# Kernel optimization log

Measured on AMD Instinct MI355X. Metric: run time of the kernel, lower is better.

Reference implementation:

```python
import jax, jax.numpy as jnp
import numpy as np

SIGMA = 0.1
GAMMA = 1.0 / (SIGMA * SIGMA)  # keops-style gauss kernel: exp(-|x-y|^2 / sigma^2)
B, N, D = 1, 8192, 3


def setup_inputs() -> dict:
    key = jax.random.key(0)
    k1, k2 = jax.random.split(key)
    control_points = jax.random.uniform(k1, (B, N, D), dtype=jnp.float32)
    mom = jax.random.normal(k2, (B, N, D), dtype=jnp.float32) * 0.1
    return {"mom": mom, "control_points": control_points}


def _pairwise_dist2(x, y):
    # x:[B,N,D], y:[B,M,D] -> [B,N,M] squared distances (no N x M x D intermediate)
    x2 = jnp.sum(x * x, -1)  # [B,N]
    y2 = jnp.sum(y * y, -1)  # [B,M]
    xy = jnp.einsum('bnd,bmd->bnm', x, y)
    return x2[:, :, None] + y2[:, None, :] - 2.0 * xy


def gauss_kernel(x, y, b):
    # K(x,y) b : [B,N,d]
    K = jnp.exp(-GAMMA * _pairwise_dist2(x, y))  # [B,N,M]
    return jnp.einsum('bnm,bmd->bnd', K, b)


def gauss_grad_kernel(p, x):
    # dH/dx_i = sum_j d/dx_i[exp(-g|x_i-x_j|^2)] <p_i,p_j>
    #         = -2g * sum_j K_ij <p_i,p_j> (x_i - x_j)
    K = jnp.exp(-GAMMA * _pairwise_dist2(x, x))        # [B,N,N]
    W = K * jnp.einsum('bnd,bmd->bnm', p, p)           # [B,N,N] weighted by <p_i,p_j>
    row_sum = jnp.sum(W, -1)                           # [B,N]
    Wx = jnp.einsum('bnm,bmd->bnd', W, x)              # [B,N,D]
    return (-2.0 * GAMMA) * (x * row_sum[:, :, None] - Wx)


def reference(mom, control_points):
    # variational_evolve: (dp/dt, dx/dt)
    dmom = -gauss_grad_kernel(mom, control_points)
    dx = gauss_kernel(control_points, control_points, mom)
    return (dmom, dx)
```

## Files before the change

### kernel.cpp

```cpp
#include <hip/hip_runtime.h>


#define TPB 256
#define ITILE 2
constexpr float GAMMA_C = 100.0f;
constexpr float LOG2E_C = 1.4426950408889634f;
constexpr float SB_C    = 2.0f * GAMMA_C * LOG2E_C;
constexpr float SC_C    = -GAMMA_C * LOG2E_C;
constexpr float LN2_C   = 0.69314718055994531f;

__global__ __launch_bounds__(TPB, 4) void lddmm_partial(
    const float* __restrict__ mom, const float* __restrict__ xpt,
    float* __restrict__ ws, int N, int SEG, int JT) {
  extern __shared__ float4 smem[];
  float4* sA = smem;
  float4* sP = smem + JT;
  const int tid = threadIdx.x;
  const int seg = blockIdx.y;

  for (int t = tid; t < JT; t += TPB) {
    const int j = seg * JT + t;
    const float bx = xpt[3*j], by = xpt[3*j+1], bz = xpt[3*j+2];
    sA[t] = make_float4(SB_C*bx, SB_C*by, SB_C*bz,
                        SC_C * fmaf(bx, bx, fmaf(by, by, bz*bz)));
    sP[t] = make_float4(mom[3*j], mom[3*j+1], mom[3*j+2], 0.f);
  }
  __syncthreads();

  const int i0 = blockIdx.x * (TPB * ITILE) + tid;
  const int i1 = i0 + TPB;

  const float x0 = xpt[3*i0], y0 = xpt[3*i0+1], z0 = xpt[3*i0+2];
  const float p0x = mom[3*i0], p0y = mom[3*i0+1], p0z = mom[3*i0+2];
  const float c0 = SC_C * fmaf(x0, x0, fmaf(y0, y0, z0*z0));
  const float x1 = xpt[3*i1], y1 = xpt[3*i1+1], z1 = xpt[3*i1+2];
  const float p1x = mom[3*i1], p1y = mom[3*i1+1], p1z = mom[3*i1+2];
  const float c1 = SC_C * fmaf(x1, x1, fmaf(y1, y1, z1*z1));

  float a0=0.f, wx0=0.f, wy0=0.f, wz0=0.f, gx0=0.f, gy0=0.f, gz0=0.f;
  float a1=0.f, wx1=0.f, wy1=0.f, wz1=0.f, gx1=0.f, gy1=0.f, gz1=0.f;

#pragma unroll 4
  for (int t = 0; t < JT; ++t) {
    const float4 A = sA[t];
    const float4 P = sP[t];
    {
      const float arg = fmaf(A.x, x0, fmaf(A.y, y0, fmaf(A.z, z0, c0 + A.w)));
      const float K   = __builtin_amdgcn_exp2f(arg);
      const float dot = fmaf(P.x, p0x, fmaf(P.y, p0y, P.z * p0z));
      const float w   = K * dot;
      a0 += w;
      wx0 = fmaf(w, A.x, wx0); wy0 = fmaf(w, A.y, wy0); wz0 = fmaf(w, A.z, wz0);
      gx0 = fmaf(K, P.x, gx0); gy0 = fmaf(K, P.y, gy0); gz0 = fmaf(K, P.z, gz0);
    }
    {
      const float arg = fmaf(A.x, x1, fmaf(A.y, y1, fmaf(A.z, z1, c1 + A.w)));
      const float K   = __builtin_amdgcn_exp2f(arg);
      const float dot = fmaf(P.x, p1x, fmaf(P.y, p1y, P.z * p1z));
      const float w   = K * dot;
      a1 += w;
      wx1 = fmaf(w, A.x, wx1); wy1 = fmaf(w, A.y, wy1); wz1 = fmaf(w, A.z, wz1);
      gx1 = fmaf(K, P.x, gx1); gy1 = fmaf(K, P.y, gy1); gz1 = fmaf(K, P.z, gz1);
    }
  }

  const size_t SN = (size_t)SEG * N;
  float* p = ws + (size_t)seg * N;
  p[0*SN+i0] = a0;  p[0*SN+i1] = a1;
  p[1*SN+i0] = wx0; p[1*SN+i1] = wx1;
  p[2*SN+i0] = wy0; p[2*SN+i1] = wy1;
  p[3*SN+i0] = wz0; p[3*SN+i1] = wz1;
  p[4*SN+i0] = gx0; p[4*SN+i1] = gx1;
  p[5*SN+i0] = gy0; p[5*SN+i1] = gy1;
  p[6*SN+i0] = gz0; p[6*SN+i1] = gz1;
}

__global__ __launch_bounds__(TPB) void lddmm_reduce(
    const float* __restrict__ ws, float* __restrict__ R, int N, int SEG) {
  const int i = blockIdx.x * TPB + threadIdx.x;
  const int c = blockIdx.y;
  const float* src = ws + (size_t)c * SEG * N + i;
  float s0 = 0.f, s1 = 0.f, s2 = 0.f, s3 = 0.f;
  int s = 0;
  for (; s + 4 <= SEG; s += 4) {
    s0 += src[(size_t)(s+0)*N]; s1 += src[(size_t)(s+1)*N];
    s2 += src[(size_t)(s+2)*N]; s3 += src[(size_t)(s+3)*N];
  }
  for (; s < SEG; ++s) s0 += src[(size_t)s*N];
  R[(size_t)c * N + i] = (s0 + s1) + (s2 + s3);
}

__global__ __launch_bounds__(TPB) void lddmm_finalize(
    const float* __restrict__ R, const float* __restrict__ xpt,
    float* __restrict__ out, int N) {
  const int i = blockIdx.x * TPB + threadIdx.x;
  const float A  = R[i];
  const float WX = R[(size_t)1*N+i], WY = R[(size_t)2*N+i], WZ = R[(size_t)3*N+i];
  const float GX = R[(size_t)4*N+i], GY = R[(size_t)5*N+i], GZ = R[(size_t)6*N+i];
  const float xi = xpt[3*i], yi = xpt[3*i+1], zi = xpt[3*i+2];
  const float TGA = 2.0f * GAMMA_C * A;
  out[3*i+0] = fmaf(TGA, xi, -LN2_C * WX);
  out[3*i+1] = fmaf(TGA, yi, -LN2_C * WY);
  out[3*i+2] = fmaf(TGA, zi, -LN2_C * WZ);
  out[3*N + 3*i + 0] = GX;
  out[3*N + 3*i + 1] = GY;
  out[3*N + 3*i + 2] = GZ;
}

__global__ __launch_bounds__(TPB) void lddmm_atomic(
    const float* __restrict__ mom, const float* __restrict__ xpt,
    float* __restrict__ out, int N) {
  const int i  = blockIdx.x * TPB + threadIdx.x;
  const int jb = blockIdx.y * TPB;
  __shared__ float4 sA[TPB], sP[TPB];
  {
    const int j = jb + threadIdx.x;
    const float bx = xpt[3*j], by = xpt[3*j+1], bz = xpt[3*j+2];
    sA[threadIdx.x] = make_float4(SB_C*bx, SB_C*by, SB_C*bz,
                                  SC_C * fmaf(bx, bx, fmaf(by, by, bz*bz)));
    sP[threadIdx.x] = make_float4(mom[3*j], mom[3*j+1], mom[3*j+2], 0.f);
  }
  __syncthreads();
  const float xi = xpt[3*i], yi = xpt[3*i+1], zi = xpt[3*i+2];
  const float pxi = mom[3*i], pyi = mom[3*i+1], pzi = mom[3*i+2];
  const float ci = SC_C * fmaf(xi, xi, fmaf(yi, yi, zi*zi));
  float a=0.f, wx=0.f, wy=0.f, wz=0.f, gx=0.f, gy=0.f, gz=0.f;
#pragma unroll 4
  for (int t = 0; t < TPB; ++t) {
    const float4 A = sA[t], P = sP[t];
    const float arg = fmaf(A.x, xi, fmaf(A.y, yi, fmaf(A.z, zi, ci + A.w)));
    const float K   = __builtin_amdgcn_exp2f(arg);
    const float dot = fmaf(P.x, pxi, fmaf(P.y, pyi, P.z * pzi));
    const float w   = K * dot;
    a += w;
    wx = fmaf(w, A.x, wx); wy = fmaf(w, A.y, wy); wz = fmaf(w, A.z, wz);
    gx = fmaf(K, P.x, gx); gy = fmaf(K, P.y, gy); gz = fmaf(K, P.z, gz);
  }
  const float TGA = 2.0f * GAMMA_C * a;
  atomicAdd(&out[3*i+0], fmaf(TGA, xi, -LN2_C * wx));
  atomicAdd(&out[3*i+1], fmaf(TGA, yi, -LN2_C * wy));
  atomicAdd(&out[3*i+2], fmaf(TGA, zi, -LN2_C * wz));
  atomicAdd(&out[3*N+3*i+0], gx);
  atomicAdd(&out[3*N+3*i+1], gy);
  atomicAdd(&out[3*N+3*i+2], gz);
}

extern "C" void kernel_launch(void* const* d_in, const int* in_sizes, int n_in,
                              void* d_out, int out_size, void* d_ws, size_t ws_size,
                              hipStream_t stream) {
  const float* mom = (const float*)d_in[0];
  const float* xpt = (const float*)d_in[1];
  float* out = (float*)d_out;
  const int N = in_sizes[0] / 3;

  auto need = [&](int s) { return (size_t)(7*s + 7) * (size_t)N * sizeof(float); };
  int SEG = 64;
  while (SEG > 2 && need(SEG) > ws_size) SEG >>= 1;

  if (need(SEG) <= ws_size) {
    const int JT = N / SEG;
    float* wsf = (float*)d_ws;
    float* R   = wsf + (size_t)7 * SEG * N;
    const size_t shmem = (size_t)JT * 2 * sizeof(float4);
    dim3 gA(N / (TPB * ITILE), SEG);
    lddmm_partial<<<gA, TPB, shmem, stream>>>(mom, xpt, wsf, N, SEG, JT);
    dim3 gB(N / TPB, 7);
    lddmm_reduce<<<gB, TPB, 0, stream>>>(wsf, R, N, SEG);
    lddmm_finalize<<<N / TPB, TPB, 0, stream>>>(R, xpt, out, N);
  } else {
    hipMemsetAsync(d_out, 0, (size_t)out_size * sizeof(float), stream);
    dim3 grid(N / TPB, N / TPB);
    lddmm_atomic<<<grid, TPB, 0, stream>>>(mom, xpt, out, N);
  }
}
```

Baseline: 97.04 us.

## Precompute packed point tables once and read them from global instead of LDS

Adds a pre-pass kernel that builds the scaled position/norm and momentum float4 tables once in workspace. The partial kernel drops its per-block LDS staging and barrier and reads these tables directly through the cache with uniform addresses. SEG is raised to 128 and launch bounds to 8 waves per SIMD to increase occupancy. The cost is an extra kernel launch, a larger partial-sum workspace and reduction, and inner-loop operands that now come from global/scalar loads instead of LDS.

Result: slower. 104.9 us (+8.1%).

```diff
diff --git a/kernel.cpp b/kernel.cpp
--- a/kernel.cpp
+++ b/kernel.cpp
@@ -9,23 +9,25 @@
 constexpr float SC_C    = -GAMMA_C * LOG2E_C;
 constexpr float LN2_C   = 0.69314718055994531f;
 
-__global__ __launch_bounds__(TPB, 4) void lddmm_partial(
+__global__ __launch_bounds__(TPB) void lddmm_pre(
+    const float* __restrict__ mom, const float* __restrict__ xpt,
+    float4* __restrict__ At, float4* __restrict__ Pt, int N) {
+  const int j = blockIdx.x * TPB + threadIdx.x;
+  if (j < N) {
+    const float bx = xpt[3*j], by = xpt[3*j+1], bz = xpt[3*j+2];
+    At[j] = make_float4(SB_C*bx, SB_C*by, SB_C*bz,
+                        SC_C * fmaf(bx, bx, fmaf(by, by, bz*bz)));
+    Pt[j] = make_float4(mom[3*j], mom[3*j+1], mom[3*j+2], 0.f);
+  }
+}
+
+__global__ __launch_bounds__(TPB, 8) void lddmm_partial(
+    const float4* __restrict__ At, const float4* __restrict__ Pt,
     const float* __restrict__ mom, const float* __restrict__ xpt,
     float* __restrict__ ws, int N, int SEG, int JT) {
-  extern __shared__ float4 smem[];
-  float4* sA = smem;
-  float4* sP = smem + JT;
   const int tid = threadIdx.x;
   const int seg = blockIdx.y;
-
-  for (int t = tid; t < JT; t += TPB) {
-    const int j = seg * JT + t;
-    const float bx = xpt[3*j], by = xpt[3*j+1], bz = xpt[3*j+2];
-    sA[t] = make_float4(SB_C*bx, SB_C*by, SB_C*bz,
-                        SC_C * fmaf(bx, bx, fmaf(by, by, bz*bz)));
-    sP[t] = make_float4(mom[3*j], mom[3*j+1], mom[3*j+2], 0.f);
-  }
-  __syncthreads();
+  const int jb  = seg * JT;
 
   const int i0 = blockIdx.x * (TPB * ITILE) + tid;
   const int i1 = i0 + TPB;
@@ -42,8 +44,8 @@
 
 #pragma unroll 4
   for (int t = 0; t < JT; ++t) {
-    const float4 A = sA[t];
-    const float4 P = sP[t];
+    const float4 A = At[jb + t];
+    const float4 P = Pt[jb + t];
     {
       const float arg = fmaf(A.x, x0, fmaf(A.y, y0, fmaf(A.z, z0, c0 + A.w)));
       const float K   = __builtin_amdgcn_exp2f(arg);
@@ -153,17 +155,22 @@
   float* out = (float*)d_out;
   const int N = in_sizes[0] / 3;
 
-  auto need = [&](int s) { return (size_t)(7*s + 7) * (size_t)N * sizeof(float); };
-  int SEG = 64;
+  auto need = [&](int s) {
+    return (size_t)(8 + 7*s + 7) * (size_t)N * sizeof(float);
+  };
+  int SEG = 128;
   while (SEG > 2 && need(SEG) > ws_size) SEG >>= 1;
 
   if (need(SEG) <= ws_size) {
     const int JT = N / SEG;
-    float* wsf = (float*)d_ws;
-    float* R   = wsf + (size_t)7 * SEG * N;
-    const size_t shmem = (size_t)JT * 2 * sizeof(float4);
+    float4* At = (float4*)d_ws;
+    float4* Pt = At + N;
+    float*  wsf = (float*)(Pt + N);
+    float*  R   = wsf + (size_t)7 * SEG * N;
+
+    lddmm_pre<<<N / TPB, TPB, 0, stream>>>(mom, xpt, At, Pt, N);
     dim3 gA(N / (TPB * ITILE), SEG);
-    lddmm_partial<<<gA, TPB, shmem, stream>>>(mom, xpt, wsf, N, SEG, JT);
+    lddmm_partial<<<gA, TPB, 0, stream>>>(At, Pt, mom, xpt, wsf, N, SEG, JT);
     dim3 gB(N / TPB, 7);
     lddmm_reduce<<<gB, TPB, 0, stream>>>(wsf, R, N, SEG);
     lddmm_finalize<<<N / TPB, TPB, 0, stream>>>(R, xpt, out, N);
```

## Broadcast source points via readlane instead of LDS and widen i-tile to four

Applied to the files above, without the earlier changes.

The partial kernel no longer stages the j-points in shared memory. Each lane of a wavefront loads one j-point into registers, and the loop broadcasts it to the whole wave with readlane across 64 iterations, removing LDS traffic and the block barrier. Each thread now accumulates four i-points instead of two, for more instruction-level parallelism and more reuse of each broadcast. The cost is fixing the segment count at N/64, which doubles the partial-sum workspace and the traffic the reduce kernel must read. If the workspace is too small for that, the code falls back to the slow atomic path.

Measured after the change: 108.0 us. 11.3% more time.

```diff
diff --git a/kernel.cpp b/kernel.cpp
--- a/kernel.cpp
+++ b/kernel.cpp
@@ -2,77 +2,101 @@
 
 
 #define TPB 256
-#define ITILE 2
+#define ITILE 4
 constexpr float GAMMA_C = 100.0f;
 constexpr float LOG2E_C = 1.4426950408889634f;
 constexpr float SB_C    = 2.0f * GAMMA_C * LOG2E_C;
 constexpr float SC_C    = -GAMMA_C * LOG2E_C;
 constexpr float LN2_C   = 0.69314718055994531f;
 
+static __device__ __forceinline__ float rl(float v, int l) {
+  return __int_as_float(__builtin_amdgcn_readlane(__float_as_int(v), l));
+}
+
 __global__ __launch_bounds__(TPB, 4) void lddmm_partial(
     const float* __restrict__ mom, const float* __restrict__ xpt,
-    float* __restrict__ ws, int N, int SEG, int JT) {
-  extern __shared__ float4 smem[];
-  float4* sA = smem;
-  float4* sP = smem + JT;
-  const int tid = threadIdx.x;
-  const int seg = blockIdx.y;
+    float* __restrict__ ws, int N, int SEG) {
+  const int tid  = threadIdx.x;
+  const int lane = tid & 63;
+  const int seg  = blockIdx.y;
+  const int j    = seg * 64 + lane;
 
-  for (int t = tid; t < JT; t += TPB) {
-    const int j = seg * JT + t;
-    const float bx = xpt[3*j], by = xpt[3*j+1], bz = xpt[3*j+2];
-    sA[t] = make_float4(SB_C*bx, SB_C*by, SB_C*bz,
-                        SC_C * fmaf(bx, bx, fmaf(by, by, bz*bz)));
-    sP[t] = make_float4(mom[3*j], mom[3*j+1], mom[3*j+2], 0.f);
-  }
-  __syncthreads();
+  const float bx = xpt[3*j], by = xpt[3*j+1], bz = xpt[3*j+2];
+  const float ax = SB_C * bx, ay = SB_C * by, az = SB_C * bz;
+  const float ac = SC_C * fmaf(bx, bx, fmaf(by, by, bz * bz));
+  const float qx = mom[3*j], qy = mom[3*j+1], qz = mom[3*j+2];
 
   const int i0 = blockIdx.x * (TPB * ITILE) + tid;
-  const int i1 = i0 + TPB;
-
+  const int i1 = i0 + TPB, i2 = i0 + 2*TPB, i3 = i0 + 3*TPB;
   const float x0 = xpt[3*i0], y0 = xpt[3*i0+1], z0 = xpt[3*i0+2];
+  const float x1 = xpt[3*i1], y1 = xpt[3*i1+1], z1 = xpt[3*i1+2];
+  const float x2 = xpt[3*i2], y2 = xpt[3*i2+1], z2 = xpt[3*i2+2];
+  const float x3 = xpt[3*i3], y3 = xpt[3*i3+1], z3 = xpt[3*i3+2];
   const float p0x = mom[3*i0], p0y = mom[3*i0+1], p0z = mom[3*i0+2];
+  const float p1x = mom[3*i1], p1y = mom[3*i1+1], p1z = mom[3*i1+2];
+  const float p2x = mom[3*i2], p2y = mom[3*i2+1], p2z = mom[3*i2+2];
+  const float p3x = mom[3*i3], p3y = mom[3*i3+1], p3z = mom[3*i3+2];
   const float c0 = SC_C * fmaf(x0, x0, fmaf(y0, y0, z0*z0));
-  const float x1 = xpt[3*i1], y1 = xpt[3*i1+1], z1 = xpt[3*i1+2];
-  const float p1x = mom[3*i1], p1y = mom[3*i1+1], p1z = mom[3*i1+2];
   const float c1 = SC_C * fmaf(x1, x1, fmaf(y1, y1, z1*z1));
+  const float c2 = SC_C * fmaf(x2, x2, fmaf(y2, y2, z2*z2));
+  const float c3 = SC_C * fmaf(x3, x3, fmaf(y3, y3, z3*z3));
 
   float a0=0.f, wx0=0.f, wy0=0.f, wz0=0.f, gx0=0.f, gy0=0.f, gz0=0.f;
   float a1=0.f, wx1=0.f, wy1=0.f, wz1=0.f, gx1=0.f, gy1=0.f, gz1=0.f;
+  float a2=0.f, wx2=0.f, wy2=0.f, wz2=0.f, gx2=0.f, gy2=0.f, gz2=0.f;
+  float a3=0.f, wx3=0.f, wy3=0.f, wz3=0.f, gx3=0.f, gy3=0.f, gz3=0.f;
 
-#pragma unroll 4
-  for (int t = 0; t < JT; ++t) {
-    const float4 A = sA[t];
-    const float4 P = sP[t];
+#pragma unroll 8
+  for (int l = 0; l < 64; ++l) {
+    const float Ax = rl(ax, l), Ay = rl(ay, l), Az = rl(az, l), Aw = rl(ac, l);
+    const float Px = rl(qx, l), Py = rl(qy, l), Pz = rl(qz, l);
     {
-      const float arg = fmaf(A.x, x0, fmaf(A.y, y0, fmaf(A.z, z0, c0 + A.w)));
+      const float arg = fmaf(Ax, x0, fmaf(Ay, y0, fmaf(Az, z0, c0 + Aw)));
       const float K   = __builtin_amdgcn_exp2f(arg);
-      const float dot = fmaf(P.x, p0x, fmaf(P.y, p0y, P.z * p0z));
+      const float dot = fmaf(Px, p0x, fmaf(Py, p0y, Pz * p0z));
       const float w   = K * dot;
       a0 += w;
-      wx0 = fmaf(w, A.x, wx0); wy0 = fmaf(w, A.y, wy0); wz0 = fmaf(w, A.z, wz0);
-      gx0 = fmaf(K, P.x, gx0); gy0 = fmaf(K, P.y, gy0); gz0 = fmaf(K, P.z, gz0);
+      wx0 = fmaf(w, Ax, wx0); wy0 = fmaf(w, Ay, wy0); wz0 = fmaf(w, Az, wz0);
+      gx0 = fmaf(K, Px, gx0); gy0 = fmaf(K, Py, gy0); gz0 = fmaf(K, Pz, gz0);
     }
     {
-      const float arg = fmaf(A.x, x1, fmaf(A.y, y1, fmaf(A.z, z1, c1 + A.w)));
+      const float arg = fmaf(Ax, x1, fmaf(Ay, y1, fmaf(Az, z1, c1 + Aw)));
       const float K   = __builtin_amdgcn_exp2f(arg);
-      const float dot = fmaf(P.x, p1x, fmaf(P.y, p1y, P.z * p1z));
+      const float dot = fmaf(Px, p1x, fmaf(Py, p1y, Pz * p1z));
       const float w   = K * dot;
       a1 += w;
-      wx1 = fmaf(w, A.x, wx1); wy1 = fmaf(w, A.y, wy1); wz1 = fmaf(w, A.z, wz1);
-      gx1 = fmaf(K, P.x, gx1); gy1 = fmaf(K, P.y, gy1); gz1 = fmaf(K, P.z, gz1);
+      wx1 = fmaf(w, Ax, wx1); wy1 = fmaf(w, Ay, wy1); wz1 = fmaf(w, Az, wz1);
+      gx1 = fmaf(K, Px, gx1); gy1 = fmaf(K, Py, gy1); gz1 = fmaf(K, Pz, gz1);
+    }
+    {
+      const float arg = fmaf(Ax, x2, fmaf(Ay, y2, fmaf(Az, z2, c2 + Aw)));
+      const float K   = __builtin_amdgcn_exp2f(arg);
+      const float dot = fmaf(Px, p2x, fmaf(Py, p2y, Pz * p2z));
+      const float w   = K * dot;
+      a2 += w;
+      wx2 = fmaf(w, Ax, wx2); wy2 = fmaf(w, Ay, wy2); wz2 = fmaf(w, Az, wz2);
+      gx2 = fmaf(K, Px, gx2); gy2 = fmaf(K, Py, gy2); gz2 = fmaf(K, Pz, gz2);
+    }
+    {
+      const float arg = fmaf(Ax, x3, fmaf(Ay, y3, fmaf(Az, z3, c3 + Aw)));
+      const float K   = __builtin_amdgcn_exp2f(arg);
+      const float dot = fmaf(Px, p3x, fmaf(Py, p3y, Pz * p3z));
+      const float w   = K * dot;
+      a3 += w;
+      wx3 = fmaf(w, Ax, wx3); wy3 = fmaf(w, Ay, wy3); wz3 = fmaf(w, Az, wz3);
+      gx3 = fmaf(K, Px, gx3); gy3 = fmaf(K, Py, gy3); gz3 = fmaf(K, Pz, gz3);
     }
   }
 
   const size_t SN = (size_t)SEG * N;
   float* p = ws + (size_t)seg * N;
-  p[0*SN+i0] = a0;  p[0*SN+i1] = a1;
-  p[1*SN+i0] = wx0; p[1*SN+i1] = wx1;
-  p[2*SN+i0] = wy0; p[2*SN+i1] = wy1;
-  p[3*SN+i0] = wz0; p[3*SN+i1] = wz1;
-  p[4*SN+i0] = gx0; p[4*SN+i1] = gx1;
-  p[5*SN+i0] = gy0; p[5*SN+i1] = gy1;
-  p[6*SN+i0] = gz0; p[6*SN+i1] = gz1;
+  p[0*SN+i0]=a0;  p[0*SN+i1]=a1;  p[0*SN+i2]=a2;  p[0*SN+i3]=a3;
+  p[1*SN+i0]=wx0; p[1*SN+i1]=wx1; p[1*SN+i2]=wx2; p[1*SN+i3]=wx3;
+  p[2*SN+i0]=wy0; p[2*SN+i1]=wy1; p[2*SN+i2]=wy2; p[2*SN+i3]=wy3;
+  p[3*SN+i0]=wz0; p[3*SN+i1]=wz1; p[3*SN+i2]=wz2; p[3*SN+i3]=wz3;
+  p[4*SN+i0]=gx0; p[4*SN+i1]=gx1; p[4*SN+i2]=gx2; p[4*SN+i3]=gx3;
+  p[5*SN+i0]=gy0; p[5*SN+i1]=gy1; p[5*SN+i2]=gy2; p[5*SN+i3]=gy3;
+  p[6*SN+i0]=gz0; p[6*SN+i1]=gz1; p[6*SN+i2]=gz2; p[6*SN+i3]=gz3;
 }
 
 __global__ __launch_bounds__(TPB) void lddmm_reduce(
@@ -153,17 +177,14 @@
   float* out = (float*)d_out;
   const int N = in_sizes[0] / 3;
 
-  auto need = [&](int s) { return (size_t)(7*s + 7) * (size_t)N * sizeof(float); };
-  int SEG = 64;
-  while (SEG > 2 && need(SEG) > ws_size) SEG >>= 1;
+  const int SEG = N / 64;
+  const size_t need = (size_t)(7*SEG + 7) * (size_t)N * sizeof(float);
 
-  if (need(SEG) <= ws_size) {
-    const int JT = N / SEG;
+  if (need <= ws_size) {
     float* wsf = (float*)d_ws;
     float* R   = wsf + (size_t)7 * SEG * N;
-    const size_t shmem = (size_t)JT * 2 * sizeof(float4);
     dim3 gA(N / (TPB * ITILE), SEG);
-    lddmm_partial<<<gA, TPB, shmem, stream>>>(mom, xpt, wsf, N, SEG, JT);
+    lddmm_partial<<<gA, TPB, 0, stream>>>(mom, xpt, wsf, N, SEG);
     dim3 gB(N / TPB, 7);
     lddmm_reduce<<<gB, TPB, 0, stream>>>(wsf, R, N, SEG);
     lddmm_finalize<<<N / TPB, TPB, 0, stream>>>(R, xpt, out, N);
```
